# Kernel optimization log

Measured on AMD Instinct MI355X. Metric: run time of the kernel, lower is better.

## Reference

```python
import jax, jax.numpy as jnp
import numpy as np
from jax import lax

B, T, E, H = 256, 512, 256, 256

def setup_inputs() -> dict:
    key = jax.random.key(0)
    k1, k2, k3, k4, k5 = jax.random.split(key, 5)
    s_in = 1.0 / np.sqrt(E)
    s_h = 1.0 / np.sqrt(H)
    return {
        "x": jax.random.normal(k1, (B, T, E), dtype=jnp.float32),
        "Wx_w": jax.random.normal(k2, (H, E), dtype=jnp.float32) * s_in,
        "Wx_b": jax.random.normal(k3, (H,), dtype=jnp.float32) * s_in,
        "Wh_w": jax.random.normal(k4, (H, H), dtype=jnp.float32) * s_h,
        "Wh_b": jax.random.normal(k5, (H,), dtype=jnp.float32) * s_h,
    }

def reference(x, Wx_w, Wx_b, Wh_w, Wh_b):
    # Precompute input gates for all timesteps: g = sigmoid(Wx(x))  [B,T,H]
    gates = jax.nn.sigmoid(jnp.einsum("bte,he->bth", x, Wx_w) + Wx_b)
    h0 = jnp.zeros((x.shape[0], Wh_w.shape[0]), dtype=x.dtype)

    def step(h, g_t):  # g_t: [B,H]
        h_new = h * g_t + (1.0 - g_t) * jnp.tanh(h @ Wh_w.T + Wh_b)
        return h_new, h_new

    _, outs = lax.scan(step, h0, jnp.swapaxes(gates, 0, 1))  # [T,B,H]
    return jnp.swapaxes(outs, 0, 1)  # [B,T,H]
```

## Files before the change

kernel.cpp:

```cpp
#include <hip/hip_runtime.h>

#define Tsz 512
#define Hsz 256

typedef __attribute__((ext_vector_type(8))) short short8;
typedef __attribute__((ext_vector_type(4))) short short4v;
typedef __attribute__((ext_vector_type(4))) float f32x4;

static __device__ __forceinline__ unsigned short f2bf(float f) {
    union { float f; unsigned int i; } v; v.f = f;
    unsigned int r = v.i + 0x7fffu + ((v.i >> 16) & 1u);
    return (unsigned short)(r >> 16);
}
static __device__ __forceinline__ short8 ld8f(const float* p) {
    const float4* q = (const float4*)p;
    float4 a = q[0], b = q[1];
    short8 v;
    v[0] = (short)f2bf(a.x); v[1] = (short)f2bf(a.y); v[2] = (short)f2bf(a.z); v[3] = (short)f2bf(a.w);
    v[4] = (short)f2bf(b.x); v[5] = (short)f2bf(b.y); v[6] = (short)f2bf(b.z); v[7] = (short)f2bf(b.w);
    return v;
}
static __device__ __forceinline__ float sigm(float z) {
    return __builtin_amdgcn_rcpf(1.f + __expf(-z));
}

__global__ __launch_bounds__(512, 1) void mgu_fused(
    const float* __restrict__ x,   const float* __restrict__ Wxw,
    const float* __restrict__ Wxb, const float* __restrict__ Whw,
    const float* __restrict__ Whb, float* __restrict__ out)
{
    __shared__ __align__(16) unsigned short xs[2][16 * 256];
    __shared__ __align__(16) float          gs[2][16 * 256];
    __shared__ __align__(16) unsigned short hbuf[2][256];

    const int tid  = threadIdx.x;
    const int b    = blockIdx.x;
    const int l    = tid & 63;
    const int w    = tid >> 6;
    const int lo16 = l & 15;
    const int hi   = l >> 4;

    short8 wfh[2][8], wfx[2][8];
    float  bh[2], bx[2];
#pragma unroll
    for (int nt = 0; nt < 2; ++nt) {
        int n = w * 32 + nt * 16 + lo16;
        bh[nt] = Whb[n];
        bx[nt] = Wxb[n];
#pragma unroll
        for (int ks = 0; ks < 8; ++ks) {
            wfh[nt][ks] = ld8f(Whw + (size_t)n * 256 + ks * 32 + hi * 8);
            wfx[nt][ks] = ld8f(Wxw + (size_t)n * 256 + ks * 32 + hi * 8);
        }
    }

    const float* xrow = x   + (size_t)b * Tsz * Hsz;
    float*       orow = out + (size_t)b * Tsz * Hsz;

#pragma unroll
    for (int i = 0; i < 4; ++i) {
        int idx = tid + i * 512;
        int m   = idx >> 6;
        int j   = idx & 63;
        float4 v = *(const float4*)(xrow + (size_t)m * 256 + j * 4);
        short4v s4;
        s4[0] = (short)f2bf(v.x); s4[1] = (short)f2bf(v.y);
        s4[2] = (short)f2bf(v.z); s4[3] = (short)f2bf(v.w);
        int r   = m & 15;
        int byt = r * 512 + (((j >> 1) ^ (r & 7)) << 4) + (j & 1) * 8;
        *(short4v*)((char*)xs[m >> 4] + byt) = s4;
    }
    if (tid < 256) hbuf[0][tid] = 0;
    __syncthreads();

    {
        f32x4 ag0 = {0.f, 0.f, 0.f, 0.f}, ag1 = {0.f, 0.f, 0.f, 0.f};
#pragma unroll
        for (int ks = 0; ks < 8; ++ks) {
            short8 afg = *(const short8*)((const char*)xs[0]
                           + lo16 * 512 + (((ks * 4 + hi) ^ (lo16 & 7)) << 4));
            ag0 = __builtin_amdgcn_mfma_f32_16x16x32_bf16(afg, wfx[0][ks], ag0, 0, 0, 0);
            ag1 = __builtin_amdgcn_mfma_f32_16x16x32_bf16(afg, wfx[1][ks], ag1, 0, 0, 0);
        }
#pragma unroll
        for (int r = 0; r < 4; ++r) {
            gs[0][(hi * 4 + r) * 256 + w * 32 + lo16]      = sigm(ag0[r] + bx[0]);
            gs[0][(hi * 4 + r) * 256 + w * 32 + 16 + lo16] = sigm(ag1[r] + bx[1]);
        }
    }

    float  hreg = 0.f;
    float4 xcarry;
    if (tid < 64) xcarry = *(const float4*)(xrow + (size_t)32 * 256 + tid * 4);

    f32x4 accg[2];
    { f32x4 z = {0.f, 0.f, 0.f, 0.f}; accg[0] = z; accg[1] = z; }

    int p = 0;
    for (int c = 0; c < 32; ++c) {
        unsigned short* xs_rd = xs[(c & 1) ^ 1];
        unsigned short* xs_wr = xs[c & 1];
        const float*    gs_rd = gs[c & 1];
        float*          gs_wr = gs[(c & 1) ^ 1];
        short8 afg;
#pragma unroll
        for (int s = 0; s < 16; ++s) {
            const int t = c * 16 + s;
            __syncthreads();

            short8 afh[8];
#pragma unroll
            for (int ks = 0; ks < 8; ++ks)
                afh[ks] = *(const short8*)(const void*)(&hbuf[p][ks * 32 + hi * 8]);

            f32x4 a0lo = {bh[0], 0.f, 0.f, 0.f}, a0hi = {0.f, 0.f, 0.f, 0.f};
            f32x4 a1lo = {bh[1], 0.f, 0.f, 0.f}, a1hi = {0.f, 0.f, 0.f, 0.f};
#pragma unroll
            for (int ks = 0; ks < 4; ++ks) {
                a0lo = __builtin_amdgcn_mfma_f32_16x16x32_bf16(afh[ks],     wfh[0][ks],     a0lo, 0, 0, 0);
                a1lo = __builtin_amdgcn_mfma_f32_16x16x32_bf16(afh[ks],     wfh[1][ks],     a1lo, 0, 0, 0);
                a0hi = __builtin_amdgcn_mfma_f32_16x16x32_bf16(afh[ks + 4], wfh[0][ks + 4], a0hi, 0, 0, 0);
                a1hi = __builtin_amdgcn_mfma_f32_16x16x32_bf16(afh[ks + 4], wfh[1][ks + 4], a1hi, 0, 0, 0);
            }

            if ((s & 1) == 0)
                afg = *(const short8*)((const char*)xs_rd
                        + lo16 * 512 + ((((s >> 1) * 4 + hi) ^ (lo16 & 7)) << 4));
            accg[s & 1] = __builtin_amdgcn_mfma_f32_16x16x32_bf16(afg, wfx[s & 1][s >> 1], accg[s & 1], 0, 0, 0);

            if (tid < 64) {
                short4v s4;
                s4[0] = (short)f2bf(xcarry.x); s4[1] = (short)f2bf(xcarry.y);
                s4[2] = (short)f2bf(xcarry.z); s4[3] = (short)f2bf(xcarry.w);
                int byt = s * 512 + (((tid >> 1) ^ (s & 7)) << 4) + (tid & 1) * 8;
                *(short4v*)((char*)xs_wr + byt) = s4;
                int nr = t + 33; if (nr > Tsz - 1) nr = Tsz - 1;
                xcarry = *(const float4*)(xrow + (size_t)nr * 256 + tid * 4);
            }

            float zz = (hi == 0) ? (a0lo[0] + a0hi[0]) : (a1lo[0] + a1hi[0]);
            zz = fminf(fmaxf(zz, -15.f), 15.f);
            float ex = __expf(2.f * zz);
            float th = (ex - 1.f) * __builtin_amdgcn_rcpf(ex + 1.f);
            if (hi < 2) {
                int   n  = w * 32 + hi * 16 + lo16;
                float g  = gs_rd[s * 256 + n];
                float hn = g * hreg + (1.f - g) * th;
                hreg = hn;
                hbuf[p ^ 1][n] = f2bf(hn);
                orow[(size_t)t * 256 + n] = hn;
            }

            if (s == 15) {
#pragma unroll
                for (int r = 0; r < 4; ++r) {
                    gs_wr[(hi * 4 + r) * 256 + w * 32 + lo16]      = sigm(accg[0][r] + bx[0]);
                    gs_wr[(hi * 4 + r) * 256 + w * 32 + 16 + lo16] = sigm(accg[1][r] + bx[1]);
                }
                f32x4 z = {0.f, 0.f, 0.f, 0.f}; accg[0] = z; accg[1] = z;
            }
            p ^= 1;
        }
    }
}

extern "C" void kernel_launch(void* const* d_in, const int* in_sizes, int n_in,
                              void* d_out, int out_size, void* d_ws, size_t ws_size,
                              hipStream_t stream) {
    const float* x   = (const float*)d_in[0];
    const float* Wxw = (const float*)d_in[1];
    const float* Wxb = (const float*)d_in[2];
    const float* Whw = (const float*)d_in[3];
    const float* Whb = (const float*)d_in[4];

    mgu_fused<<<dim3(256), dim3(512), 0, stream>>>(x, Wxw, Wxb, Whw, Whb, (float*)d_out);
}
```

Before: 272.9 us.

## Split recurrence and input-gate GEMM into separate warp groups with priority

The block grows to 1024 threads. Warps 0-7 run only the serial recurrent scan, and warps 8-15 compute the input-gate GEMM chunks and stream x into shared memory. Each warp now holds only one weight matrix in registers, and the scan warps raise their scheduling priority around the recurrent MFMAs so the critical path competes less with the gate work. The cost is twice as many warps taking part in every per-step barrier, plus possible register-limit pressure at the larger block size.

Measured after the change: 416.3 us. 1.53x slower.

```diff
diff --git a/kernel.cpp b/kernel.cpp
--- a/kernel.cpp
+++ b/kernel.cpp
@@ -24,7 +24,7 @@
     return __builtin_amdgcn_rcpf(1.f + __expf(-z));
 }
 
-__global__ __launch_bounds__(512, 1) void mgu_fused(
+__global__ __launch_bounds__(1024, 1) void mgu_fused(
     const float* __restrict__ x,   const float* __restrict__ Wxw,
     const float* __restrict__ Wxb, const float* __restrict__ Whw,
     const float* __restrict__ Whb, float* __restrict__ out)
@@ -37,29 +37,30 @@
     const int b    = blockIdx.x;
     const int l    = tid & 63;
     const int w    = tid >> 6;
+    const int wg   = w & 7;
     const int lo16 = l & 15;
     const int hi   = l >> 4;
+    const bool is_scan = (w < 8);
 
-    short8 wfh[2][8], wfx[2][8];
-    float  bh[2], bx[2];
+    const float* Wsel = is_scan ? Whw : Wxw;
+    const float* Bsel = is_scan ? Whb : Wxb;
+    short8 wf[2][8];
+    float  bb[2];
 #pragma unroll
     for (int nt = 0; nt < 2; ++nt) {
-        int n = w * 32 + nt * 16 + lo16;
-        bh[nt] = Whb[n];
-        bx[nt] = Wxb[n];
+        int n = wg * 32 + nt * 16 + lo16;
+        bb[nt] = Bsel[n];
 #pragma unroll
-        for (int ks = 0; ks < 8; ++ks) {
-            wfh[nt][ks] = ld8f(Whw + (size_t)n * 256 + ks * 32 + hi * 8);
-            wfx[nt][ks] = ld8f(Wxw + (size_t)n * 256 + ks * 32 + hi * 8);
-        }
+        for (int ks = 0; ks < 8; ++ks)
+            wf[nt][ks] = ld8f(Wsel + (size_t)n * 256 + ks * 32 + hi * 8);
     }
 
     const float* xrow = x   + (size_t)b * Tsz * Hsz;
     float*       orow = out + (size_t)b * Tsz * Hsz;
 
 #pragma unroll
-    for (int i = 0; i < 4; ++i) {
-        int idx = tid + i * 512;
+    for (int i = 0; i < 2; ++i) {
+        int idx = tid + i * 1024;
         int m   = idx >> 6;
         int j   = idx & 63;
         float4 v = *(const float4*)(xrow + (size_t)m * 256 + j * 4);
@@ -73,91 +74,94 @@
     if (tid < 256) hbuf[0][tid] = 0;
     __syncthreads();
 
-    {
+    if (!is_scan) {
         f32x4 ag0 = {0.f, 0.f, 0.f, 0.f}, ag1 = {0.f, 0.f, 0.f, 0.f};
 #pragma unroll
         for (int ks = 0; ks < 8; ++ks) {
-            short8 afg = *(const short8*)((const char*)xs[0]
-                           + lo16 * 512 + (((ks * 4 + hi) ^ (lo16 & 7)) << 4));
-            ag0 = __builtin_amdgcn_mfma_f32_16x16x32_bf16(afg, wfx[0][ks], ag0, 0, 0, 0);
-            ag1 = __builtin_amdgcn_mfma_f32_16x16x32_bf16(afg, wfx[1][ks], ag1, 0, 0, 0);
+            short8 a = *(const short8*)((const char*)xs[0]
+                         + lo16 * 512 + (((ks * 4 + hi) ^ (lo16 & 7)) << 4));
+            ag0 = __builtin_amdgcn_mfma_f32_16x16x32_bf16(a, wf[0][ks], ag0, 0, 0, 0);
+            ag1 = __builtin_amdgcn_mfma_f32_16x16x32_bf16(a, wf[1][ks], ag1, 0, 0, 0);
         }
 #pragma unroll
         for (int r = 0; r < 4; ++r) {
-            gs[0][(hi * 4 + r) * 256 + w * 32 + lo16]      = sigm(ag0[r] + bx[0]);
-            gs[0][(hi * 4 + r) * 256 + w * 32 + 16 + lo16] = sigm(ag1[r] + bx[1]);
+            gs[0][(hi * 4 + r) * 256 + wg * 32 + lo16]      = sigm(ag0[r] + bb[0]);
+            gs[0][(hi * 4 + r) * 256 + wg * 32 + 16 + lo16] = sigm(ag1[r] + bb[1]);
         }
     }
 
     float  hreg = 0.f;
     float4 xcarry;
-    if (tid < 64) xcarry = *(const float4*)(xrow + (size_t)32 * 256 + tid * 4);
+    if (w == 8) xcarry = *(const float4*)(xrow + (size_t)32 * 256 + l * 4);
 
-    f32x4 accg[2];
-    { f32x4 z = {0.f, 0.f, 0.f, 0.f}; accg[0] = z; accg[1] = z; }
+    f32x4 accg0 = {0.f, 0.f, 0.f, 0.f}, accg1 = {0.f, 0.f, 0.f, 0.f};
+    short8 afg;
+    int p = 0;
 
-    int p = 0;
     for (int c = 0; c < 32; ++c) {
         unsigned short* xs_rd = xs[(c & 1) ^ 1];
         unsigned short* xs_wr = xs[c & 1];
         const float*    gs_rd = gs[c & 1];
         float*          gs_wr = gs[(c & 1) ^ 1];
-        short8 afg;
 #pragma unroll
         for (int s = 0; s < 16; ++s) {
             const int t = c * 16 + s;
             __syncthreads();
 
-            short8 afh[8];
+            if (is_scan) {
+                __builtin_amdgcn_s_setprio(1);
+                f32x4 a0lo = {bb[0], 0.f, 0.f, 0.f}, a0hi = {0.f, 0.f, 0.f, 0.f};
+                f32x4 a1lo = {bb[1], 0.f, 0.f, 0.f}, a1hi = {0.f, 0.f, 0.f, 0.f};
 #pragma unroll
-            for (int ks = 0; ks < 8; ++ks)
-                afh[ks] = *(const short8*)(const void*)(&hbuf[p][ks * 32 + hi * 8]);
+                for (int ks = 0; ks < 4; ++ks) {
+                    short8 afA = *(const short8*)(const void*)(&hbuf[p][ks * 32 + hi * 8]);
+                    short8 afB = *(const short8*)(const void*)(&hbuf[p][(ks + 4) * 32 + hi * 8]);
+                    a0lo = __builtin_amdgcn_mfma_f32_16x16x32_bf16(afA, wf[0][ks],     a0lo, 0, 0, 0);
+                    a1lo = __builtin_amdgcn_mfma_f32_16x16x32_bf16(afA, wf[1][ks],     a1lo, 0, 0, 0);
+                    a0hi = __builtin_amdgcn_mfma_f32_16x16x32_bf16(afB, wf[0][ks + 4], a0hi, 0, 0, 0);
+                    a1hi = __builtin_amdgcn_mfma_f32_16x16x32_bf16(afB, wf[1][ks + 4], a1hi, 0, 0, 0);
+                }
+                __builtin_amdgcn_s_setprio(0);
 
-            f32x4 a0lo = {bh[0], 0.f, 0.f, 0.f}, a0hi = {0.f, 0.f, 0.f, 0.f};
-            f32x4 a1lo = {bh[1], 0.f, 0.f, 0.f}, a1hi = {0.f, 0.f, 0.f, 0.f};
+                float zz = (hi == 0) ? (a0lo[0] + a0hi[0]) : (a1lo[0] + a1hi[0]);
+                zz = fminf(fmaxf(zz, -15.f), 15.f);
+                float ex = __expf(2.f * zz);
+                float th = (ex - 1.f) * __builtin_amdgcn_rcpf(ex + 1.f);
+                if (hi < 2) {
+                    int   n  = wg * 32 + hi * 16 + lo16;
+                    float g  = gs_rd[s * 256 + n];
+                    float hn = g * hreg + (1.f - g) * th;
+                    hreg = hn;
+                    hbuf[p ^ 1][n] = f2bf(hn);
+                    orow[(size_t)t * 256 + n] = hn;
+                }
+            } else {
+                if ((s & 1) == 0)
+                    afg = *(const short8*)((const char*)xs_rd
+                            + lo16 * 512 + ((((s >> 1) * 4 + hi) ^ (lo16 & 7)) << 4));
+                if ((s & 1) == 0)
+                    accg0 = __builtin_amdgcn_mfma_f32_16x16x32_bf16(afg, wf[0][s >> 1], accg0, 0, 0, 0);
+                else
+                    accg1 = __builtin_amdgcn_mfma_f32_16x16x32_bf16(afg, wf[1][s >> 1], accg1, 0, 0, 0);
+
+                if (w == 8) {
+                    short4v s4;
+                    s4[0] = (short)f2bf(xcarry.x); s4[1] = (short)f2bf(xcarry.y);
+                    s4[2] = (short)f2bf(xcarry.z); s4[3] = (short)f2bf(xcarry.w);
+                    int byt = s * 512 + (((l >> 1) ^ (s & 7)) << 4) + (l & 1) * 8;
+                    *(short4v*)((char*)xs_wr + byt) = s4;
+                    int nr = t + 33; if (nr > Tsz - 1) nr = Tsz - 1;
+                    xcarry = *(const float4*)(xrow + (size_t)nr * 256 + l * 4);
+                }
+
+                if (s == 15) {
 #pragma unroll
-            for (int ks = 0; ks < 4; ++ks) {
-                a0lo = __builtin_amdgcn_mfma_f32_16x16x32_bf16(afh[ks],     wfh[0][ks],     a0lo, 0, 0, 0);
-                a1lo = __builtin_amdgcn_mfma_f32_16x16x32_bf16(afh[ks],     wfh[1][ks],     a1lo, 0, 0, 0);
-                a0hi = __builtin_amdgcn_mfma_f32_16x16x32_bf16(afh[ks + 4], wfh[0][ks + 4], a0hi, 0, 0, 0);
-                a1hi = __builtin_amdgcn_mfma_f32_16x16x32_bf16(afh[ks + 4], wfh[1][ks + 4], a1hi, 0, 0, 0);
-            }
-
-            if ((s & 1) == 0)
-                afg = *(const short8*)((const char*)xs_rd
-                        + lo16 * 512 + ((((s >> 1) * 4 + hi) ^ (lo16 & 7)) << 4));
-            accg[s & 1] = __builtin_amdgcn_mfma_f32_16x16x32_bf16(afg, wfx[s & 1][s >> 1], accg[s & 1], 0, 0, 0);
-
-            if (tid < 64) {
-                short4v s4;
-                s4[0] = (short)f2bf(xcarry.x); s4[1] = (short)f2bf(xcarry.y);
-                s4[2] = (short)f2bf(xcarry.z); s4[3] = (short)f2bf(xcarry.w);
-                int byt = s * 512 + (((tid >> 1) ^ (s & 7)) << 4) + (tid & 1) * 8;
-                *(short4v*)((char*)xs_wr + byt) = s4;
-                int nr = t + 33; if (nr > Tsz - 1) nr = Tsz - 1;
-                xcarry = *(const float4*)(xrow + (size_t)nr * 256 + tid * 4);
-            }
-
-            float zz = (hi == 0) ? (a0lo[0] + a0hi[0]) : (a1lo[0] + a1hi[0]);
-            zz = fminf(fmaxf(zz, -15.f), 15.f);
-            float ex = __expf(2.f * zz);
-            float th = (ex - 1.f) * __builtin_amdgcn_rcpf(ex + 1.f);
-            if (hi < 2) {
-                int   n  = w * 32 + hi * 16 + lo16;
-                float g  = gs_rd[s * 256 + n];
-                float hn = g * hreg + (1.f - g) * th;
-                hreg = hn;
-                hbuf[p ^ 1][n] = f2bf(hn);
-                orow[(size_t)t * 256 + n] = hn;
-            }
-
-            if (s == 15) {
-#pragma unroll
-                for (int r = 0; r < 4; ++r) {
-                    gs_wr[(hi * 4 + r) * 256 + w * 32 + lo16]      = sigm(accg[0][r] + bx[0]);
-                    gs_wr[(hi * 4 + r) * 256 + w * 32 + 16 + lo16] = sigm(accg[1][r] + bx[1]);
+                    for (int r = 0; r < 4; ++r) {
+                        gs_wr[(hi * 4 + r) * 256 + wg * 32 + lo16]      = sigm(accg0[r] + bb[0]);
+                        gs_wr[(hi * 4 + r) * 256 + wg * 32 + 16 + lo16] = sigm(accg1[r] + bb[1]);
+                    }
+                    f32x4 z = {0.f, 0.f, 0.f, 0.f}; accg0 = z; accg1 = z;
                 }
-                f32x4 z = {0.f, 0.f, 0.f, 0.f}; accg[0] = z; accg[1] = z;
             }
             p ^= 1;
         }
@@ -173,5 +177,5 @@
     const float* Whw = (const float*)d_in[3];
     const float* Whb = (const float*)d_in[4];
 
-    mgu_fused<<<dim3(256), dim3(512), 0, stream>>>(x, Wxw, Wxb, Whw, Whb, (float*)d_out);
+    mgu_fused<<<dim3(256), dim3(1024), 0, stream>>>(x, Wxw, Wxb, Whw, Whb, (float*)d_out);
 }
```
